# Kernel optimization log

Measured on AMD Instinct MI355X. Metric: run time of the kernel, lower is better.

The kernel has to match this reference:

```python
import math
import jax, jax.numpy as jnp
import numpy as np

W_BITS = 8
A_BITS = 8
N_HEADS = 16

def fake_quant(x, bits):
    # symmetric per-tensor fake quantization with straight-through estimator
    if bits >= 32:
        return x
    qmax = float(2 ** (bits - 1) - 1)
    scale = jnp.maximum(jnp.max(jnp.abs(x)) / qmax, 1e-8)
    q = jnp.round(x / scale) * scale
    return x + jax.lax.stop_gradient(q - x)

def qlinear(x, W, b):
    # QuantizeLinear: quantize activations (a_bits) and weights (w_bits), then y = x @ W^T + b
    xq = fake_quant(x, A_BITS)
    Wq = fake_quant(W, W_BITS)
    return jnp.einsum('bsd,ed->bse', xq, Wq) + b

def setup_inputs() -> dict:
    key = jax.random.key(0)
    B, S, D = 2, 2048, 1024
    ks = jax.random.split(key, 6)
    inp = {
        'hidden_states': jax.random.normal(ks[0], (B, S, D), dtype=jnp.float32),
        'attention_mask': jnp.ones((B, S), dtype=jnp.float32),
        'Wq': 0.02 * jax.random.normal(ks[1], (D, D), dtype=jnp.float32),
        'bq': jnp.zeros((D,), dtype=jnp.float32),
        'Wk': 0.02 * jax.random.normal(ks[2], (D, D), dtype=jnp.float32),
        'bk': jnp.zeros((D,), dtype=jnp.float32),
        'Wv': 0.02 * jax.random.normal(ks[3], (D, D), dtype=jnp.float32),
        'bv': jnp.zeros((D,), dtype=jnp.float32),
        'Wo': 0.02 * jax.random.normal(ks[4], (D, D), dtype=jnp.float32),
        'bo': jnp.zeros((D,), dtype=jnp.float32),
    }
    return inp

def reference(hidden_states, attention_mask, Wq, bq, Wk, bk, Wv, bv, Wo, bo):
    B, S, D = hidden_states.shape
    H = N_HEADS
    hd = D // H

    q = qlinear(hidden_states, Wq, bq).reshape(B, S, H, hd)
    k = qlinear(hidden_states, Wk, bk).reshape(B, S, H, hd)
    v = qlinear(hidden_states, Wv, bv).reshape(B, S, H, hd)

    # scores: [B, H, Sq, Sk]
    scores = jnp.einsum('bqhd,bkhd->bhqk', q, k) / math.sqrt(hd)
    mask_bias = (1.0 - attention_mask)[:, None, None, :] * -10000.0
    scores = scores + mask_bias
    probs = jax.nn.softmax(scores, axis=-1)

    attn = jnp.einsum('bhqk,bkhd->bqhd', probs, v).reshape(B, S, D)
    return qlinear(attn, Wo, bo)
```

## Files before the change

### kernel.cpp

```cpp
#include <hip/hip_runtime.h>
#include <cstddef>
#include <cstdint>

constexpr int Bb = 2, Ss = 2048, Dd = 1024, Hh = 16, HD = 64;
constexpr int Mm = Bb * Ss;

typedef int v4i __attribute__((ext_vector_type(4)));
typedef __bf16 bf16x8 __attribute__((ext_vector_type(8)));
typedef __bf16 bf16x2 __attribute__((ext_vector_type(2)));
typedef float f32x16 __attribute__((ext_vector_type(16)));

#define QPOSTMUL 0.18033688f

__device__ __forceinline__ float qscale(float amax) {
    return fmaxf(amax / 127.0f, 1e-8f);
}

__device__ __forceinline__ unsigned short bf16rtn(float x) {
    __bf16 b = (__bf16)x;
    return __builtin_bit_cast(unsigned short, b);
}

__device__ __forceinline__ unsigned pack_bf16x2(float a, float b) {
    bf16x2 h;
    h[0] = (__bf16)a;
    h[1] = (__bf16)b;
    return __builtin_bit_cast(unsigned, h);
}

__global__ void amax_all(const float4* __restrict__ hidden,
                         const float4* __restrict__ w0, const float4* __restrict__ w1,
                         const float4* __restrict__ w2, const float4* __restrict__ w3,
                         unsigned* __restrict__ slots) {
    const float4* src; int n4, slot, bx, nb;
    if (blockIdx.x < 448) { src = hidden; n4 = Mm * Dd / 4; slot = 0; bx = blockIdx.x; nb = 448; }
    else {
        int w = (blockIdx.x - 448) >> 4; bx = (blockIdx.x - 448) & 15; nb = 16;
        src = w == 0 ? w0 : w == 1 ? w1 : w == 2 ? w2 : w3;
        n4 = Dd * Dd / 4; slot = 1 + w;
    }
    float m = 0.f;
    for (int i = bx * blockDim.x + threadIdx.x; i < n4; i += nb * blockDim.x) {
        float4 v = src[i];
        m = fmaxf(m, fmaxf(fmaxf(fabsf(v.x), fabsf(v.y)), fmaxf(fabsf(v.z), fabsf(v.w))));
    }
    #pragma unroll
    for (int off = 32; off > 0; off >>= 1) m = fmaxf(m, __shfl_down(m, off, 64));
    __shared__ float sm[4];
    int lane = threadIdx.x & 63, wid = threadIdx.x >> 6;
    if (lane == 0) sm[wid] = m;
    __syncthreads();
    if (threadIdx.x == 0) {
        float mm = fmaxf(fmaxf(sm[0], sm[1]), fmaxf(sm[2], sm[3]));
        atomicMax(slots + slot, __float_as_uint(mm));
    }
}

__global__ void quant_all(const float* __restrict__ hidden,
                          const float* __restrict__ w0, const float* __restrict__ w1,
                          const float* __restrict__ w2, const float* __restrict__ w3,
                          const float* __restrict__ amax,
                          char* __restrict__ hq8, char* __restrict__ Wall8) {
    const float* x; char* y; int n4, slot, bx, nb;
    if (blockIdx.x < 1024) { x = hidden; y = hq8; n4 = Mm * Dd / 4; slot = 0; bx = blockIdx.x; nb = 1024; }
    else {
        int w = (blockIdx.x - 1024) >> 5; bx = (blockIdx.x - 1024) & 31; nb = 32;
        x = w == 0 ? w0 : w == 1 ? w1 : w == 2 ? w2 : w3;
        y = Wall8 + ((size_t)w << 20);
        n4 = Dd * Dd / 4; slot = 1 + w;
    }
    float s = qscale(amax[slot]);
    const float4* x4 = (const float4*)x;
    char4* y4 = (char4*)y;
    for (int i = bx * blockDim.x + threadIdx.x; i < n4; i += nb * blockDim.x) {
        float4 v = x4[i];
        char4 q;
        q.x = (char)(int)rintf(v.x / s);
        q.y = (char)(int)rintf(v.y / s);
        q.z = (char)(int)rintf(v.z / s);
        q.w = (char)(int)rintf(v.w / s);
        y4[i] = q;
    }
}

__global__ void quant_a(const float* __restrict__ x, char* __restrict__ y,
                        const float* __restrict__ amax, int n4) {
    float s = qscale(amax[0]);
    int stride = gridDim.x * blockDim.x;
    const float4* x4 = (const float4*)x;
    char4* y4 = (char4*)y;
    for (int i = blockIdx.x * blockDim.x + threadIdx.x; i < n4; i += stride) {
        float4 v = x4[i];
        char4 q;
        q.x = (char)(int)rintf(v.x / s);
        q.y = (char)(int)rintf(v.y / s);
        q.z = (char)(int)rintf(v.z / s);
        q.w = (char)(int)rintf(v.w / s);
        y4[i] = q;
    }
}

#define GLOAD_LDS16(g, l) __builtin_amdgcn_global_load_lds( \
    (const __attribute__((address_space(1))) unsigned int*)(g), \
    (__attribute__((address_space(3))) unsigned int*)(l), 16, 0, 0)

__device__ __forceinline__ void gemm128_core(const char* __restrict__ A, const char* __restrict__ Bw,
                                             int bm, int bn, int K, int t,
                                             char* At, char* Bt, v4i acc[4][4]) {
    const int lane = t & 63, w = t >> 6;
    const int wm = (w >> 1) * 64, wn = (w & 1) * 64;
    const int lr = lane & 15, kq = lane >> 4;
    const int rs = w * 16 + (lane >> 2);
    const int cc = lane & 3;

    for (int k0 = 0; k0 < K; k0 += 64) {
        __syncthreads();
        #pragma unroll
        for (int h = 0; h < 2; h++) {
            int r = rs + h * 64;
            int cs = cc ^ ((r >> 1) & 3);
            GLOAD_LDS16(A  + (size_t)(bm + r) * K + k0 + cs * 16, At + r * 64 + cc * 16);
            GLOAD_LDS16(Bw + (size_t)(bn + r) * K + k0 + cs * 16, Bt + r * 64 + cc * 16);
        }
        __syncthreads();

        v4i af[4], bf[4];
        #pragma unroll
        for (int mt = 0; mt < 4; mt++) {
            int row = wm + mt * 16 + lr;
            af[mt] = *(const v4i*)(At + row * 64 + ((kq ^ ((row >> 1) & 3)) << 4));
        }
        #pragma unroll
        for (int nt = 0; nt < 4; nt++) {
            int row = wn + nt * 16 + lr;
            bf[nt] = *(const v4i*)(Bt + row * 64 + ((kq ^ ((row >> 1) & 3)) << 4));
        }
        #pragma unroll
        for (int mt = 0; mt < 4; mt++)
            #pragma unroll
            for (int nt = 0; nt < 4; nt++)
                acc[mt][nt] = __builtin_amdgcn_mfma_i32_16x16x64_i8(af[mt], bf[nt], acc[mt][nt], 0, 0, 0);
    }
}

__global__ __launch_bounds__(256) void gemm_qkv(const char* __restrict__ A,
                                                const char* __restrict__ Wall8,
                                                const float* __restrict__ bq,
                                                const float* __restrict__ bk,
                                                const float* __restrict__ bv,
                                                const float* __restrict__ amax,
                                                unsigned short* __restrict__ qb16,
                                                unsigned short* __restrict__ kb16,
                                                unsigned short* __restrict__ vt16) {
    __shared__ alignas(16) char pool[34816];
    char* At = pool;
    char* Bt = pool + 8192;
    unsigned short (*Tt)[136] = (unsigned short(*)[136])pool;

    const int t = threadIdx.x, lane = t & 63, w = t >> 6;
    const int mat = blockIdx.x >> 3;
    const int bn = (blockIdx.x & 7) * 128, bm = blockIdx.y * 128;
    const int wm = (w >> 1) * 64, wn = (w & 1) * 64;
    const int lr = lane & 15, kq = lane >> 4;

    const v4i vzero = {0, 0, 0, 0};
    v4i acc[4][4];
    #pragma unroll
    for (int mt = 0; mt < 4; mt++)
        #pragma unroll
        for (int nt = 0; nt < 4; nt++) acc[mt][nt] = vzero;

    const char* Bw = Wall8 + ((size_t)mat << 20);
    gemm128_core(A, Bw, bm, bn, Dd, t, At, Bt, acc);

    const float* bias = mat == 0 ? bq : mat == 1 ? bk : bv;
    float sc = qscale(amax[0]) * qscale(amax[1 + mat]);
    float pm = (mat == 0) ? QPOSTMUL : 1.0f;

    __syncthreads();

    if (mat != 2) {
        #pragma unroll
        for (int nt = 0; nt < 4; nt++) {
            int n_l = wn + nt * 16 + lr;
            float bv_ = bias[bn + n_l];
            #pragma unroll
            for (int mt = 0; mt < 4; mt++) {
                int m_l = wm + mt * 16 + kq * 4;
                #pragma unroll
                for (int rg = 0; rg < 4; rg++)
                    Tt[m_l + rg][n_l] = bf16rtn(((float)acc[mt][nt][rg] * sc + bv_) * pm);
            }
        }
    } else {
        #pragma unroll
        for (int nt = 0; nt < 4; nt++) {
            int n_l = wn + nt * 16 + lr;
            float bv_ = bias[bn + n_l];
            #pragma unroll
            for (int mt = 0; mt < 4; mt++) {
                int m_l = wm + mt * 16 + kq * 4;
                ushort4 hv;
                hv.x = bf16rtn((float)acc[mt][nt][0] * sc + bv_);
                hv.y = bf16rtn((float)acc[mt][nt][1] * sc + bv_);
                hv.z = bf16rtn((float)acc[mt][nt][2] * sc + bv_);
                hv.w = bf16rtn((float)acc[mt][nt][3] * sc + bv_);
                *(ushort4*)&Tt[n_l][m_l] = hv;
            }
        }
    }
    __syncthreads();

    {
        int row = t >> 1, half = t & 1;
        unsigned short* dst;
        if (mat != 2) {
            dst = (mat == 0 ? qb16 : kb16) + (size_t)(bm + row) * Dd + bn + half * 64;
        } else {
            int n = bn + row;
            int e = n & 63, hc = n >> 6;
            int b_ = bm >> 11, s_ = (bm & 2047) + half * 64;
            dst = vt16 + (((size_t)(b_ * Hh + hc) * 64 + e) * Ss) + s_;
        }
        const unsigned short* srcl = &Tt[row][half * 64];
        #pragma unroll
        for (int c = 0; c < 8; c++)
            *(int4*)(dst + c * 8) = *(const int4*)(srcl + c * 8);
    }
}

__global__ __launch_bounds__(256) void gemm_o(const char* __restrict__ A,
                                              const char* __restrict__ Bw,
                                              const float* __restrict__ bias,
                                              const float* __restrict__ amaxA,
                                              const float* __restrict__ amaxB,
                                              float* __restrict__ C) {
    __shared__ alignas(16) char At[128 * 64];
    __shared__ alignas(16) char Bt[64 * 64];
    const int t = threadIdx.x, lane = t & 63, w = t >> 6;
    const int bn = blockIdx.x * 64, bm = blockIdx.y * 128;
    const int wm = (w >> 1) * 64, wn = (w & 1) * 32;
    const int lr = lane & 15, kq = lane >> 4;
    const int rs = t >> 2, cc = t & 3;
    const int cs = cc ^ ((rs >> 1) & 3);
    const int rs2 = rs + 64, cs2 = cc ^ ((rs2 >> 1) & 3);

    const v4i vzero = {0, 0, 0, 0};
    v4i acc[4][2];
    #pragma unroll
    for (int mt = 0; mt < 4; mt++) { acc[mt][0] = vzero; acc[mt][1] = vzero; }

    for (int k0 = 0; k0 < Dd; k0 += 64) {
        __syncthreads();
        GLOAD_LDS16(A  + (size_t)(bm + rs)  * Dd + k0 + cs  * 16, At + rs  * 64 + cc * 16);
        GLOAD_LDS16(A  + (size_t)(bm + rs2) * Dd + k0 + cs2 * 16, At + rs2 * 64 + cc * 16);
        GLOAD_LDS16(Bw + (size_t)(bn + rs)  * Dd + k0 + cs  * 16, Bt + rs  * 64 + cc * 16);
        __syncthreads();

        v4i af[4], bf[2];
        #pragma unroll
        for (int mt = 0; mt < 4; mt++) {
            int row = wm + mt * 16 + lr;
            af[mt] = *(const v4i*)(At + row * 64 + ((kq ^ ((row >> 1) & 3)) << 4));
        }
        #pragma unroll
        for (int nt = 0; nt < 2; nt++) {
            int row = wn + nt * 16 + lr;
            bf[nt] = *(const v4i*)(Bt + row * 64 + ((kq ^ ((row >> 1) & 3)) << 4));
        }
        #pragma unroll
        for (int mt = 0; mt < 4; mt++)
            #pragma unroll
            for (int nt = 0; nt < 2; nt++)
                acc[mt][nt] = __builtin_amdgcn_mfma_i32_16x16x64_i8(af[mt], bf[nt], acc[mt][nt], 0, 0, 0);
    }

    float sc = qscale(amaxA[0]) * qscale(amaxB[0]);
    #pragma unroll
    for (int nt = 0; nt < 2; nt++) {
        int n = bn + wn + nt * 16 + lr;
        float bv_ = bias[n];
        #pragma unroll
        for (int mt = 0; mt < 4; mt++)
            #pragma unroll
            for (int rg = 0; rg < 4; rg++) {
                int m = bm + wm + mt * 16 + kq * 4 + rg;
                C[(size_t)m * Dd + n] = (float)acc[mt][nt][rg] * sc + bv_;
            }
    }
}

__global__ __launch_bounds__(512, 4) void attn_mfma(
    const unsigned short* __restrict__ qb16, const unsigned short* __restrict__ kb16,
    const unsigned short* __restrict__ vt16,
    const float* __restrict__ mask, float* __restrict__ Ob, unsigned* __restrict__ amax_out) {
    __shared__ alignas(16) char apool[36864];
    unsigned short (*Ks)[64][72] = (unsigned short(*)[64][72])apool;
    unsigned short (*Vs)[64][72] = (unsigned short(*)[64][72])(apool + 18432);
    __shared__ float wred[4];

    const int t = threadIdx.x, lane = t & 63, wq = t >> 6;
    const int g = wq >> 2, wq4 = wq & 3, tg = t & 255;
    const int ln31 = lane & 31, h5 = lane >> 5;
    const int b = blockIdx.z, h = blockIdx.y, q0 = blockIdx.x * 128;
    const int kbase = g << 10;

    bf16x8 qf[4];
    {
        int qrow = q0 + wq4 * 32 + ln31;
        const unsigned short* qb_ = qb16 + ((size_t)(b * Ss + qrow)) * Dd + h * 64 + h5 * 8;
        #pragma unroll
        for (int c = 0; c < 4; c++) qf[c] = *(const bf16x8*)(qb_ + c * 16);
    }

    const int srow = tg >> 2, cp = (tg & 3) * 2;
    const int rho = (srow >> 1) + (srow & 1) * 32;
    int4 pk0, pk1, pv0, pv1; float pmv = 1.f;
    auto prefetch = [&](int k0) {
        const unsigned short* gk = kb16 + ((size_t)(b * Ss + k0 + srow)) * Dd + h * 64 + cp * 8;
        const unsigned short* gv = vt16 + (((size_t)(b * Hh + h) * 64 + srow)) * Ss + k0 + cp * 8;
        pk0 = *(const int4*)gk; pk1 = *(const int4*)(gk + 8);
        pv0 = *(const int4*)gv; pv1 = *(const int4*)(gv + 8);
        pmv = mask[b * Ss + k0 + lane];
    };

    f32x16 o0 = 0.f, o1 = 0.f;
    float la0 = 0.f, la1 = 0.f, la2 = 0.f, la3 = 0.f;

    prefetch(kbase);
    for (int k0 = kbase; k0 < kbase + Ss / 2; k0 += 64) {
        __syncthreads();
        *(int4*)&Ks[g][rho][cp * 8]      = pk0;
        *(int4*)&Ks[g][rho][cp * 8 + 8]  = pk1;
        *(int4*)&Vs[g][srow][cp * 8]     = pv0;
        *(int4*)&Vs[g][srow][cp * 8 + 8] = pv1;
        unsigned long long bm = __ballot(pmv > 0.5f);
        __syncthreads();
        if (k0 + 64 < kbase + Ss / 2) prefetch(k0 + 64);

        f32x16 sc0 = 0.f, sc1 = 0.f;
        __builtin_amdgcn_s_setprio(1);
        #pragma unroll
        for (int c = 0; c < 4; c++) {
            bf16x8 kh0 = *(const bf16x8*)&Ks[g][ln31][c * 16 + h5 * 8];
            bf16x8 kh1 = *(const bf16x8*)&Ks[g][32 + ln31][c * 16 + h5 * 8];
            sc0 = __builtin_amdgcn_mfma_f32_32x32x16_bf16(kh0, qf[c], sc0, 0, 0, 0);
            sc1 = __builtin_amdgcn_mfma_f32_32x32x16_bf16(kh1, qf[c], sc1, 0, 0, 0);
        }
        __builtin_amdgcn_s_setprio(0);

        #pragma unroll
        for (int c = 0; c < 4; c++) {
            float e0[4], e1[4];
            #pragma unroll
            for (int j = 0; j < 4; j++) {
                e0[j] = __builtin_amdgcn_exp2f(sc0[4 * c + j]);
                e1[j] = __builtin_amdgcn_exp2f(sc1[4 * c + j]);
            }
            if (bm != ~0ull) {
                #pragma unroll
                for (int j = 0; j < 4; j++) {
                    int kk = 16 * c + 8 * h5 + 2 * j;
                    e0[j] *= (float)(int)((bm >> kk) & 1);
                    e1[j] *= (float)(int)((bm >> (kk + 1)) & 1);
                }
            }
            la0 += e0[0] + e1[0];
            la1 += e0[1] + e1[1];
            la2 += e0[2] + e1[2];
            la3 += e0[3] + e1[3];

            uint4 pw;
            pw.x = pack_bf16x2(e0[0], e1[0]);
            pw.y = pack_bf16x2(e0[1], e1[1]);
            pw.z = pack_bf16x2(e0[2], e1[2]);
            pw.w = pack_bf16x2(e0[3], e1[3]);
            bf16x8 pf = __builtin_bit_cast(bf16x8, pw);
            bf16x8 vh0 = *(const bf16x8*)&Vs[g][ln31][c * 16 + h5 * 8];
            bf16x8 vh1 = *(const bf16x8*)&Vs[g][32 + ln31][c * 16 + h5 * 8];
            __builtin_amdgcn_s_setprio(1);
            o0 = __builtin_amdgcn_mfma_f32_32x32x16_bf16(pf, vh0, o0, 0, 0, 0);
            o1 = __builtin_amdgcn_mfma_f32_32x32x16_bf16(pf, vh1, o1, 0, 0, 0);
            __builtin_amdgcn_s_setprio(0);
        }
    }

    float lsum = (la0 + la1) + (la2 + la3);
    lsum += __shfl_xor(lsum, 32, 64);

    __syncthreads();
    float (*Osh)[65] = (float(*)[65])apool;
    float (*Lsh2)[128] = (float(*)[128])(apool + 33280);

    if (lane < 32) Lsh2[g][wq4 * 32 + ln31] = lsum;
    if (g == 1) {
        #pragma unroll
        for (int r = 0; r < 16; r++) {
            int rl = wq4 * 32 + (r & 3) + 8 * (r >> 2) + 4 * h5;
            Osh[rl][ln31]      = o0[r];
            Osh[rl][32 + ln31] = o1[r];
        }
    }
    __syncthreads();
    if (g == 0) {
        float lmax = 0.f;
        #pragma unroll
        for (int r = 0; r < 16; r++) {
            int rl = wq4 * 32 + (r & 3) + 8 * (r >> 2) + 4 * h5;
            float inv = 1.0f / (Lsh2[0][rl] + Lsh2[1][rl]);
            size_t ro = ((size_t)(b * Ss + q0 + rl)) * Dd + h * 64;
            float v0 = (o0[r] + Osh[rl][ln31]) * inv;
            float v1 = (o1[r] + Osh[rl][32 + ln31]) * inv;
            Ob[ro + ln31]      = v0;
            Ob[ro + 32 + ln31] = v1;
            lmax = fmaxf(lmax, fmaxf(fabsf(v0), fabsf(v1)));
        }
        #pragma unroll
        for (int off = 32; off > 0; off >>= 1) lmax = fmaxf(lmax, __shfl_xor(lmax, off, 64));
        if (lane == 0) wred[wq4] = lmax;
    }
    __syncthreads();
    if (t == 0) {
        float m = fmaxf(fmaxf(wred[0], wred[1]), fmaxf(wred[2], wred[3]));
        atomicMax(amax_out, __float_as_uint(m));
    }
}

extern "C" void kernel_launch(void* const* d_in, const int* in_sizes, int n_in,
                              void* d_out, int out_size, void* d_ws, size_t ws_size,
                              hipStream_t stream) {
    const float* hidden = (const float*)d_in[0];
    const float* mask   = (const float*)d_in[1];
    const float* Wq = (const float*)d_in[2];
    const float* bq = (const float*)d_in[3];
    const float* Wk = (const float*)d_in[4];
    const float* bk = (const float*)d_in[5];
    const float* Wv = (const float*)d_in[6];
    const float* bv = (const float*)d_in[7];
    const float* Wo = (const float*)d_in[8];
    const float* bo = (const float*)d_in[9];
    float* out = (float*)d_out;

    char* ws = (char*)d_ws;
    float* scal = (float*)ws;
    size_t off = 1024;
    const size_t szH8 = (size_t)Mm * Dd;
    const size_t szHb = (size_t)Mm * Dd * sizeof(unsigned short);
    const size_t szHf = (size_t)Mm * Dd * sizeof(float);
    char* hq8   = ws + off; off += szH8;
    char* Wall8 = ws + off; off += 4u << 20;
    char* aq8   = ws + off; off += szH8;
    unsigned short* qb16 = (unsigned short*)(ws + off); off += szHb;
    unsigned short* kb16 = (unsigned short*)(ws + off); off += szHb;
    unsigned short* vt16 = (unsigned short*)(ws + off); off += szHb;
    float* ab = (float*)(ws + off); off += szHf;

    hipMemsetAsync(scal, 0, 64, stream);

    amax_all<<<512, 256, 0, stream>>>((const float4*)hidden, (const float4*)Wq,
                                      (const float4*)Wk, (const float4*)Wv, (const float4*)Wo,
                                      (unsigned*)scal);
    quant_all<<<1152, 256, 0, stream>>>(hidden, Wq, Wk, Wv, Wo, scal, hq8, Wall8);

    gemm_qkv<<<dim3(24, 32), 256, 0, stream>>>(hq8, Wall8, bq, bk, bv, scal,
                                               qb16, kb16, vt16);

    attn_mfma<<<dim3(Ss / 128, Hh, Bb), 512, 0, stream>>>(qb16, kb16, vt16,
                                                          mask, ab, (unsigned*)(scal + 5));

    quant_a<<<1024, 256, 0, stream>>>(ab, aq8, scal + 5, Mm * Dd / 4);

    gemm_o<<<dim3(16, 32), 256, 0, stream>>>(aq8, Wall8 + (3u << 20), bo,
                                             scal + 5, scal + 4, out);
}
```

Measured before the change: 218.9 us.

## Double-buffer LDS tiles in int8 GEMMs and attention K/V loop

Adds two-stage LDS buffering to the shared int8 GEMM core, the output-projection GEMM and the attention K/V loop. Each GEMM iteration now issues the next tile's global-to-LDS copy into the alternate buffer before computing on the current one. Both GEMMs and the attention loop drop to one barrier per iteration instead of two. The cost is double the LDS footprint, which in the attention kernel (72 KB per block) may cut the number of resident blocks per CU below the launch-bounds target.

```diff
diff --git a/kernel.cpp b/kernel.cpp
--- a/kernel.cpp
+++ b/kernel.cpp
@@ -112,34 +112,47 @@
     const int lr = lane & 15, kq = lane >> 4;
     const int rs = w * 16 + (lane >> 2);
     const int cc = lane & 3;
-
-    for (int k0 = 0; k0 < K; k0 += 64) {
-        __syncthreads();
+    const int NT = K / 64;
+
+    auto stage = [&](int s, int buf) {
+        int k0 = s * 64;
+        char* Ab = At + buf * 16384;
+        char* Bb = Bt + buf * 16384;
         #pragma unroll
         for (int h = 0; h < 2; h++) {
             int r = rs + h * 64;
             int cs = cc ^ ((r >> 1) & 3);
-            GLOAD_LDS16(A  + (size_t)(bm + r) * K + k0 + cs * 16, At + r * 64 + cc * 16);
-            GLOAD_LDS16(Bw + (size_t)(bn + r) * K + k0 + cs * 16, Bt + r * 64 + cc * 16);
-        }
-        __syncthreads();
-
+            GLOAD_LDS16(A  + (size_t)(bm + r) * K + k0 + cs * 16, Ab + r * 64 + cc * 16);
+            GLOAD_LDS16(Bw + (size_t)(bn + r) * K + k0 + cs * 16, Bb + r * 64 + cc * 16);
+        }
+    };
+
+    stage(0, 0);
+    __syncthreads();
+    for (int s = 0; s < NT; s++) {
+        const int cur = s & 1;
+        if (s + 1 < NT) stage(s + 1, cur ^ 1);
+
+        const char* Ac = At + cur * 16384;
+        const char* Bc = Bt + cur * 16384;
         v4i af[4], bf[4];
         #pragma unroll
         for (int mt = 0; mt < 4; mt++) {
             int row = wm + mt * 16 + lr;
-            af[mt] = *(const v4i*)(At + row * 64 + ((kq ^ ((row >> 1) & 3)) << 4));
+            af[mt] = *(const v4i*)(Ac + row * 64 + ((kq ^ ((row >> 1) & 3)) << 4));
         }
         #pragma unroll
         for (int nt = 0; nt < 4; nt++) {
             int row = wn + nt * 16 + lr;
-            bf[nt] = *(const v4i*)(Bt + row * 64 + ((kq ^ ((row >> 1) & 3)) << 4));
+            bf[nt] = *(const v4i*)(Bc + row * 64 + ((kq ^ ((row >> 1) & 3)) << 4));
         }
         #pragma unroll
         for (int mt = 0; mt < 4; mt++)
             #pragma unroll
             for (int nt = 0; nt < 4; nt++)
                 acc[mt][nt] = __builtin_amdgcn_mfma_i32_16x16x64_i8(af[mt], bf[nt], acc[mt][nt], 0, 0, 0);
+
+        if (s + 1 < NT) __syncthreads();
     }
 }
 
@@ -235,8 +248,7 @@
                                               const float* __restrict__ amaxA,
                                               const float* __restrict__ amaxB,
                                               float* __restrict__ C) {
-    __shared__ alignas(16) char At[128 * 64];
-    __shared__ alignas(16) char Bt[64 * 64];
+    __shared__ alignas(16) char pool[24576];
     const int t = threadIdx.x, lane = t & 63, w = t >> 6;
     const int bn = blockIdx.x * 64, bm = blockIdx.y * 128;
     const int wm = (w >> 1) * 64, wn = (w & 1) * 32;
@@ -245,34 +257,47 @@
     const int cs = cc ^ ((rs >> 1) & 3);
     const int rs2 = rs + 64, cs2 = cc ^ ((rs2 >> 1) & 3);
 
+    auto stage = [&](int s, int buf) {
+        int k0 = s * 64;
+        char* Ab = pool + buf * 12288;
+        char* Bb = Ab + 8192;
+        GLOAD_LDS16(A  + (size_t)(bm + rs)  * Dd + k0 + cs  * 16, Ab + rs  * 64 + cc * 16);
+        GLOAD_LDS16(A  + (size_t)(bm + rs2) * Dd + k0 + cs2 * 16, Ab + rs2 * 64 + cc * 16);
+        GLOAD_LDS16(Bw + (size_t)(bn + rs)  * Dd + k0 + cs  * 16, Bb + rs  * 64 + cc * 16);
+    };
+
     const v4i vzero = {0, 0, 0, 0};
     v4i acc[4][2];
     #pragma unroll
     for (int mt = 0; mt < 4; mt++) { acc[mt][0] = vzero; acc[mt][1] = vzero; }
 
-    for (int k0 = 0; k0 < Dd; k0 += 64) {
-        __syncthreads();
-        GLOAD_LDS16(A  + (size_t)(bm + rs)  * Dd + k0 + cs  * 16, At + rs  * 64 + cc * 16);
-        GLOAD_LDS16(A  + (size_t)(bm + rs2) * Dd + k0 + cs2 * 16, At + rs2 * 64 + cc * 16);
-        GLOAD_LDS16(Bw + (size_t)(bn + rs)  * Dd + k0 + cs  * 16, Bt + rs  * 64 + cc * 16);
-        __syncthreads();
-
+    stage(0, 0);
+    __syncthreads();
+    const int NT = Dd / 64;
+    for (int s = 0; s < NT; s++) {
+        const int cur = s & 1;
+        if (s + 1 < NT) stage(s + 1, cur ^ 1);
+
+        const char* Ac = pool + cur * 12288;
+        const char* Bc = Ac + 8192;
         v4i af[4], bf[2];
         #pragma unroll
         for (int mt = 0; mt < 4; mt++) {
             int row = wm + mt * 16 + lr;
-            af[mt] = *(const v4i*)(At + row * 64 + ((kq ^ ((row >> 1) & 3)) << 4));
+            af[mt] = *(const v4i*)(Ac + row * 64 + ((kq ^ ((row >> 1) & 3)) << 4));
         }
         #pragma unroll
         for (int nt = 0; nt < 2; nt++) {
             int row = wn + nt * 16 + lr;
-            bf[nt] = *(const v4i*)(Bt + row * 64 + ((kq ^ ((row >> 1) & 3)) << 4));
+            bf[nt] = *(const v4i*)(Bc + row * 64 + ((kq ^ ((row >> 1) & 3)) << 4));
         }
         #pragma unroll
         for (int mt = 0; mt < 4; mt++)
             #pragma unroll
             for (int nt = 0; nt < 2; nt++)
                 acc[mt][nt] = __builtin_amdgcn_mfma_i32_16x16x64_i8(af[mt], bf[nt], acc[mt][nt], 0, 0, 0);
+
+        if (s + 1 < NT) __syncthreads();
     }
 
     float sc = qscale(amaxA[0]) * qscale(amaxB[0]);
@@ -294,9 +319,9 @@
     const unsigned short* __restrict__ qb16, const unsigned short* __restrict__ kb16,
     const unsigned short* __restrict__ vt16,
     const float* __restrict__ mask, float* __restrict__ Ob, unsigned* __restrict__ amax_out) {
-    __shared__ alignas(16) char apool[36864];
-    unsigned short (*Ks)[64][72] = (unsigned short(*)[64][72])apool;
-    unsigned short (*Vs)[64][72] = (unsigned short(*)[64][72])(apool + 18432);
+    __shared__ alignas(16) char apool[73728];
+    unsigned short (*Ks)[2][64][72] = (unsigned short(*)[2][64][72])apool;
+    unsigned short (*Vs)[2][64][72] = (unsigned short(*)[2][64][72])(apool + 36864);
     __shared__ float wred[4];
 
     const int t = threadIdx.x, lane = t & 63, wq = t >> 6;
@@ -327,23 +352,24 @@
     f32x16 o0 = 0.f, o1 = 0.f;
     float la0 = 0.f, la1 = 0.f, la2 = 0.f, la3 = 0.f;
 
+    constexpr int NT = (Ss / 2) / 64;
     prefetch(kbase);
-    for (int k0 = kbase; k0 < kbase + Ss / 2; k0 += 64) {
-        __syncthreads();
-        *(int4*)&Ks[g][rho][cp * 8]      = pk0;
-        *(int4*)&Ks[g][rho][cp * 8 + 8]  = pk1;
-        *(int4*)&Vs[g][srow][cp * 8]     = pv0;
-        *(int4*)&Vs[g][srow][cp * 8 + 8] = pv1;
+    int cur = 0;
+    for (int it = 0; it < NT; it++) {
+        *(int4*)&Ks[g][cur][rho][cp * 8]      = pk0;
+        *(int4*)&Ks[g][cur][rho][cp * 8 + 8]  = pk1;
+        *(int4*)&Vs[g][cur][srow][cp * 8]     = pv0;
+        *(int4*)&Vs[g][cur][srow][cp * 8 + 8] = pv1;
         unsigned long long bm = __ballot(pmv > 0.5f);
         __syncthreads();
-        if (k0 + 64 < kbase + Ss / 2) prefetch(k0 + 64);
+        if (it + 1 < NT) prefetch(kbase + (it + 1) * 64);
 
         f32x16 sc0 = 0.f, sc1 = 0.f;
         __builtin_amdgcn_s_setprio(1);
         #pragma unroll
         for (int c = 0; c < 4; c++) {
-            bf16x8 kh0 = *(const bf16x8*)&Ks[g][ln31][c * 16 + h5 * 8];
-            bf16x8 kh1 = *(const bf16x8*)&Ks[g][32 + ln31][c * 16 + h5 * 8];
+            bf16x8 kh0 = *(const bf16x8*)&Ks[g][cur][ln31][c * 16 + h5 * 8];
+            bf16x8 kh1 = *(const bf16x8*)&Ks[g][cur][32 + ln31][c * 16 + h5 * 8];
             sc0 = __builtin_amdgcn_mfma_f32_32x32x16_bf16(kh0, qf[c], sc0, 0, 0, 0);
             sc1 = __builtin_amdgcn_mfma_f32_32x32x16_bf16(kh1, qf[c], sc1, 0, 0, 0);
         }
@@ -376,13 +402,14 @@
             pw.z = pack_bf16x2(e0[2], e1[2]);
             pw.w = pack_bf16x2(e0[3], e1[3]);
             bf16x8 pf = __builtin_bit_cast(bf16x8, pw);
-            bf16x8 vh0 = *(const bf16x8*)&Vs[g][ln31][c * 16 + h5 * 8];
-            bf16x8 vh1 = *(const bf16x8*)&Vs[g][32 + ln31][c * 16 + h5 * 8];
+            bf16x8 vh0 = *(const bf16x8*)&Vs[g][cur][ln31][c * 16 + h5 * 8];
+            bf16x8 vh1 = *(const bf16x8*)&Vs[g][cur][32 + ln31][c * 16 + h5 * 8];
             __builtin_amdgcn_s_setprio(1);
             o0 = __builtin_amdgcn_mfma_f32_32x32x16_bf16(pf, vh0, o0, 0, 0, 0);
             o1 = __builtin_amdgcn_mfma_f32_32x32x16_bf16(pf, vh1, o1, 0, 0, 0);
             __builtin_amdgcn_s_setprio(0);
         }
+        cur ^= 1;
     }
 
     float lsum = (la0 + la1) + (la2 + la3);
```

After: 220.9 us. No clear change (+0.9%).
